# Kernel optimization log

Measured on AMD Instinct MI355X. Metric: run time of the kernel, lower is better.

Reference implementation:

```python
import jax, jax.numpy as jnp
import numpy as np

B, T, IN, OUT, R = 8, 2048, 4096, 4096, 64


def setup_inputs() -> dict:
    key = jax.random.key(0)
    ks = jax.random.split(key, 6)
    x = jax.random.normal(ks[0], (B, T, IN), dtype=jnp.float32)
    weight_main = jax.random.normal(ks[1], (OUT, IN), dtype=jnp.float32) * (1.0 / np.sqrt(IN))
    U = jax.random.normal(ks[2], (OUT, R), dtype=jnp.float32) * 0.02
    S = jax.random.uniform(ks[3], (R,), dtype=jnp.float32)
    V = jax.random.normal(ks[4], (R, IN), dtype=jnp.float32) * 0.02
    bias = jax.random.normal(ks[5], (OUT,), dtype=jnp.float32) * 0.01
    return {"x": x, "weight_main": weight_main, "U": U, "S": S, "V": V, "bias": bias}


def reference(x, weight_main, U, S, V, bias):
    # residual_weight = einsum('ij,j,jk->ik', U, S, V): full [out, in] materialization
    residual_weight = jnp.einsum('ij,j,jk->ik', U, S, V)
    weight = weight_main + residual_weight
    # F.linear: x @ weight.T + bias
    return jnp.einsum('bti,oi->bto', x, weight) + bias
```

## Files before the change

### kernel.cpp

```cpp
#include <hip/hip_runtime.h>
#include <hip/hip_bf16.h>
#include <stdint.h>

#define DI __device__ __forceinline__

typedef __attribute__((ext_vector_type(4))) float f32x4;
typedef __attribute__((ext_vector_type(8))) short bf16x8;
typedef __attribute__((ext_vector_type(4))) short s16x4;

typedef unsigned short ushort_t;

constexpr int M_ = 16384;
constexpr int N_ = 4096;
constexpr int K_ = 4096;
constexpr int R_ = 64;

constexpr int BM = 256, BN = 256, BK = 64;
constexpr int NSEG = 3;
constexpr int NT_SEG = K_ / BK;
constexpr int TOT_T = NSEG * NT_SEG;

DI ushort_t f32_to_bf16_rne(float f) {
    unsigned u = __builtin_bit_cast(unsigned, f);
    u += 0x7FFFu + ((u >> 16) & 1u);
    return (ushort_t)(u >> 16);
}
DI float bf16_to_f32(ushort_t h) {
    return __builtin_bit_cast(float, (unsigned)h << 16);
}

DI void async_cp16(const void* g, void* l) {
    __builtin_amdgcn_global_load_lds(
        (const __attribute__((address_space(1))) unsigned*)g,
        (__attribute__((address_space(3))) unsigned*)l, 16, 0, 0);
}

__global__ __launch_bounds__(256) void k_fold_us(const float* __restrict__ U,
                                                 const float* __restrict__ S,
                                                 float* __restrict__ US) {
    int i = blockIdx.x * 256 + threadIdx.x;
    if (i < N_ * R_) US[i] = U[i] * S[i & (R_ - 1)];
}

__global__ __launch_bounds__(256) void k_fuse_w(const float* __restrict__ WM,
                                                const float* __restrict__ US,
                                                const float* __restrict__ V,
                                                ushort_t* __restrict__ hiW,
                                                ushort_t* __restrict__ loW) {
    __shared__ __align__(16) float sUS[64][68];
    __shared__ __align__(16) float sV[64][128];
    int t = threadIdx.x;
    int n0 = (blockIdx.x >> 5) * 64;
    int k0 = (blockIdx.x & 31) * 128;
#pragma unroll
    for (int j = 0; j < 4; ++j) {
        int f = j * 1024 + t * 4;
        int r = f >> 6, c = f & 63;
        *(f32x4*)&sUS[r][c] = *(const f32x4*)&US[(size_t)(n0 + r) * R_ + c];
    }
#pragma unroll
    for (int j = 0; j < 8; ++j) {
        int f = j * 1024 + t * 4;
        int r = f >> 7, c = f & 127;
        *(f32x4*)&sV[r][c] = *(const f32x4*)&V[(size_t)r * K_ + k0 + c];
    }
    __syncthreads();
    int tn = t >> 5;
    int tk = t & 31;
    float acc[8][4] = {};
    for (int r = 0; r < R_; ++r) {
        f32x4 vv = *(const f32x4*)&sV[r][tk * 4];
#pragma unroll
        for (int a = 0; a < 8; ++a) {
            float u = sUS[tn * 8 + a][r];
#pragma unroll
            for (int c = 0; c < 4; ++c) acc[a][c] += u * vv[c];
        }
    }
#pragma unroll
    for (int a = 0; a < 8; ++a) {
        int n = n0 + tn * 8 + a;
        int k = k0 + tk * 4;
        f32x4 wmv = *(const f32x4*)&WM[(size_t)n * K_ + k];
        s16x4 h4, l4;
#pragma unroll
        for (int c = 0; c < 4; ++c) {
            float w = wmv[c] + acc[a][c];
            ushort_t h = f32_to_bf16_rne(w);
            h4[c] = (short)h;
            l4[c] = (short)f32_to_bf16_rne(w - bf16_to_f32(h));
        }
        *(s16x4*)&hiW[(size_t)n * K_ + k] = h4;
        *(s16x4*)&loW[(size_t)n * K_ + k] = l4;
    }
}

__global__ __launch_bounds__(256) void k_split_x(const float* __restrict__ X,
                                                 ushort_t* __restrict__ hiA,
                                                 ushort_t* __restrict__ loA) {
    size_t i = ((size_t)blockIdx.x * 256 + threadIdx.x) * 8;
    f32x4 a = *(const f32x4*)&X[i];
    f32x4 b = *(const f32x4*)&X[i + 4];
    bf16x8 h, l;
#pragma unroll
    for (int j = 0; j < 4; ++j) {
        ushort_t ha = f32_to_bf16_rne(a[j]);
        ushort_t hb = f32_to_bf16_rne(b[j]);
        h[j]     = (short)ha;
        h[4 + j] = (short)hb;
        l[j]     = (short)f32_to_bf16_rne(a[j] - bf16_to_f32(ha));
        l[4 + j] = (short)f32_to_bf16_rne(b[j] - bf16_to_f32(hb));
    }
    *(bf16x8*)&hiA[i] = h;
    *(bf16x8*)&loA[i] = l;
}

__global__ __launch_bounds__(512, 2) void k_gemm_big(const ushort_t* __restrict__ hiA,
                                                     const ushort_t* __restrict__ loA,
                                                     const ushort_t* __restrict__ hiW,
                                                     const ushort_t* __restrict__ loW,
                                                     const float* __restrict__ bias,
                                                     float* __restrict__ out) {
    __shared__ __align__(16) ushort_t lA[2][BM * BK];
    __shared__ __align__(16) ushort_t lB[2][BN * BK];

    int bid = blockIdx.x;
    int wg  = (bid & 7) * (gridDim.x >> 3) + (bid >> 3);
    int m0  = (wg >> 4) * BM;
    int n0  = (wg & 15) * BN;

    int tid  = threadIdx.x;
    int lane = tid & 63;
    int w    = tid >> 6;
    int wr   = w >> 2;
    int wc   = w & 3;
    int fr   = lane & 15;
    int fq   = lane >> 4;

    f32x4 acc[8][4] = {};

    auto stage = [&](int tau, int bsel) {
        int seg = tau >> 6;
        const ushort_t* As = (seg == 1) ? loA : hiA;
        const ushort_t* Bs = (seg == 2) ? loW : hiW;
        int k0 = (tau & (NT_SEG - 1)) * BK;
        ushort_t* la = lA[bsel];
        ushort_t* lb = lB[bsel];
#pragma unroll
        for (int j = 0; j < 4; ++j) {
            int ci = j * 512 + tid;
            int row = ci >> 3, pc = ci & 7;
            int lc  = pc ^ (row & 7);
            async_cp16(&As[(size_t)(m0 + row) * K_ + k0 + lc * 8], &la[ci * 8]);
        }
#pragma unroll
        for (int j = 0; j < 4; ++j) {
            int ci = j * 512 + tid;
            int row = ci >> 3, pc = ci & 7;
            int lc  = pc ^ (row & 7);
            async_cp16(&Bs[(size_t)(n0 + row) * K_ + k0 + lc * 8], &lb[ci * 8]);
        }
    };

    auto compute = [&](int bsel) {
        const ushort_t* la = lA[bsel];
        const ushort_t* lb = lB[bsel];
#pragma unroll
        for (int ks = 0; ks < 2; ++ks) {
            bf16x8 af[8], bf[4];
#pragma unroll
            for (int i = 0; i < 8; ++i) {
                int row = wr * 128 + i * 16 + fr;
                af[i] = *(const bf16x8*)&la[row * 64 + (((ks * 4 + fq) ^ (row & 7)) << 3)];
            }
#pragma unroll
            for (int j = 0; j < 4; ++j) {
                int row = wc * 64 + j * 16 + fr;
                bf[j] = *(const bf16x8*)&lb[row * 64 + (((ks * 4 + fq) ^ (row & 7)) << 3)];
            }
            __builtin_amdgcn_s_setprio(1);
#pragma unroll
            for (int i = 0; i < 8; ++i)
#pragma unroll
                for (int j = 0; j < 4; ++j)
                    acc[i][j] = __builtin_amdgcn_mfma_f32_16x16x32_bf16(af[i], bf[j], acc[i][j], 0, 0, 0);
            __builtin_amdgcn_s_setprio(0);
        }
    };

    stage(0, 0);
    for (int tau = 0; tau < TOT_T - 1; ++tau) {
        stage(tau + 1, (tau + 1) & 1);
        asm volatile("s_waitcnt vmcnt(8)" ::: "memory");
        __builtin_amdgcn_s_barrier();
        compute(tau & 1);
        asm volatile("" ::: "memory");
        __builtin_amdgcn_s_barrier();
        asm volatile("" ::: "memory");
    }
    asm volatile("s_waitcnt vmcnt(0)" ::: "memory");
    __builtin_amdgcn_s_barrier();
    compute((TOT_T - 1) & 1);

    float bcol[4];
#pragma unroll
    for (int j = 0; j < 4; ++j) bcol[j] = bias[n0 + wc * 64 + j * 16 + fr];
#pragma unroll
    for (int i = 0; i < 8; ++i) {
        int gm = m0 + wr * 128 + i * 16 + fq * 4;
#pragma unroll
        for (int j = 0; j < 4; ++j) {
            int gn = n0 + wc * 64 + j * 16 + fr;
#pragma unroll
            for (int r2 = 0; r2 < 4; ++r2)
                out[(size_t)(gm + r2) * N_ + gn] = acc[i][j][r2] + bcol[j];
        }
    }
}

__global__ __launch_bounds__(256, 2) void k_gemm_small(const float* __restrict__ X,
                                                       const ushort_t* __restrict__ hiW,
                                                       const ushort_t* __restrict__ loW,
                                                       const float* __restrict__ bias,
                                                       float* __restrict__ out) {
    __shared__ __align__(16) ushort_t lA[128 * 64];
    __shared__ __align__(16) ushort_t lB[128 * 64];
    int bid = blockIdx.x;
    int cpx = gridDim.x >> 3;
    int wg  = (bid & 7) * cpx + (bid >> 3);
    constexpr int NBN = N_ / 128;
    int m0 = (wg / NBN) * 128;
    int n0 = (wg % NBN) * 128;
    int tid  = threadIdx.x;
    int lane = tid & 63;
    int w    = tid >> 6;
    int wr   = w >> 1, wc = w & 1;
    int fr   = lane & 15;
    int fq   = lane >> 4;
    f32x4 acc[4][4] = {};
    for (int seg = 0; seg < 3; ++seg) {
        const ushort_t* Bs = (seg == 2) ? loW : hiW;
        bool wantLo = (seg == 1);
        for (int kt = 0; kt < K_ / 64; ++kt) {
            int k0 = kt * 64;
#pragma unroll
            for (int j = 0; j < 4; ++j) {
                int f = j * 2048 + tid * 8;
                int row = f >> 6, col = f & 63;
                async_cp16(&Bs[(size_t)(n0 + row) * K_ + k0 + col], &lB[f]);
            }
#pragma unroll
            for (int j = 0; j < 4; ++j) {
                int f = j * 2048 + tid * 8;
                int row = f >> 6, c = f & 63;
                const float* xp = &X[(size_t)(m0 + row) * K_ + k0 + c];
                f32x4 x0 = *(const f32x4*)xp;
                f32x4 x1 = *(const f32x4*)(xp + 4);
                bf16x8 o;
#pragma unroll
                for (int e = 0; e < 4; ++e) {
                    ushort_t h0 = f32_to_bf16_rne(x0[e]);
                    ushort_t h1 = f32_to_bf16_rne(x1[e]);
                    o[e]     = (short)(wantLo ? f32_to_bf16_rne(x0[e] - bf16_to_f32(h0)) : h0);
                    o[4 + e] = (short)(wantLo ? f32_to_bf16_rne(x1[e] - bf16_to_f32(h1)) : h1);
                }
                *(bf16x8*)&lA[f] = o;
            }
            __syncthreads();
#pragma unroll
            for (int ks = 0; ks < 2; ++ks) {
                bf16x8 af[4], bfv[4];
#pragma unroll
                for (int i = 0; i < 4; ++i) {
                    af[i]  = *(const bf16x8*)&lA[(wr * 64 + i * 16 + fr) * 64 + ks * 32 + fq * 8];
                    bfv[i] = *(const bf16x8*)&lB[(wc * 64 + i * 16 + fr) * 64 + ks * 32 + fq * 8];
                }
#pragma unroll
                for (int i = 0; i < 4; ++i)
#pragma unroll
                    for (int j = 0; j < 4; ++j)
                        acc[i][j] = __builtin_amdgcn_mfma_f32_16x16x32_bf16(af[i], bfv[j], acc[i][j], 0, 0, 0);
            }
            __syncthreads();
        }
    }
    float bcol[4];
#pragma unroll
    for (int j = 0; j < 4; ++j) bcol[j] = bias[n0 + wc * 64 + j * 16 + fr];
#pragma unroll
    for (int i = 0; i < 4; ++i) {
        int gm = m0 + wr * 64 + i * 16 + fq * 4;
#pragma unroll
        for (int j = 0; j < 4; ++j) {
            int gn = n0 + wc * 64 + j * 16 + fr;
#pragma unroll
            for (int r2 = 0; r2 < 4; ++r2)
                out[(size_t)(gm + r2) * N_ + gn] = acc[i][j][r2] + bcol[j];
        }
    }
}

__global__ __launch_bounds__(256) void k_naive(const float* __restrict__ X,
                                               const float* __restrict__ WM,
                                               const float* __restrict__ U,
                                               const float* __restrict__ S,
                                               const float* __restrict__ V,
                                               const float* __restrict__ bias,
                                               float* __restrict__ out) {
    __shared__ __align__(16) float sX[64][68];
    __shared__ __align__(16) float sW[64][68];
    __shared__ __align__(16) float sV[64][68];
    int t = threadIdx.x;
    int m0 = (blockIdx.x >> 6) * 64;
    int n0 = (blockIdx.x & 63) * 64;
    int tm = t >> 4, tn = t & 15;
    float acc[4][4] = {}, pacc[4][4] = {};
    for (int kc = 0; kc < K_ / 64; ++kc) {
        __syncthreads();
#pragma unroll
        for (int j = 0; j < 4; ++j) {
            int f = j * 1024 + t * 4;
            int r = f >> 6, c = f & 63;
            *(f32x4*)&sX[r][c] = *(const f32x4*)&X[(size_t)(m0 + r) * K_ + kc * 64 + c];
            *(f32x4*)&sW[r][c] = *(const f32x4*)&WM[(size_t)(n0 + r) * K_ + kc * 64 + c];
            *(f32x4*)&sV[r][c] = *(const f32x4*)&V[(size_t)r * K_ + kc * 64 + c];
        }
        __syncthreads();
        for (int k4 = 0; k4 < 16; ++k4) {
            f32x4 xa[4], wb[4], vb[4];
#pragma unroll
            for (int a = 0; a < 4; ++a) xa[a] = *(const f32x4*)&sX[tm * 4 + a][k4 * 4];
#pragma unroll
            for (int b = 0; b < 4; ++b) {
                wb[b] = *(const f32x4*)&sW[tn * 4 + b][k4 * 4];
                vb[b] = *(const f32x4*)&sV[tn * 4 + b][k4 * 4];
            }
#pragma unroll
            for (int a = 0; a < 4; ++a)
#pragma unroll
                for (int b = 0; b < 4; ++b)
#pragma unroll
                    for (int e = 0; e < 4; ++e) {
                        acc[a][b]  += xa[a][e] * wb[b][e];
                        pacc[a][b] += xa[a][e] * vb[b][e];
                    }
        }
    }
    __syncthreads();
#pragma unroll
    for (int j = 0; j < 4; ++j) {
        int f = j * 1024 + t * 4;
        int nl = f >> 6, r = f & 63;
        f32x4 uu = *(const f32x4*)&U[(size_t)(n0 + nl) * R_ + r];
        f32x4 ss = *(const f32x4*)&S[r];
        f32x4 us = uu * ss;
        *(f32x4*)&sV[nl][r] = us;
    }
#pragma unroll
    for (int a = 0; a < 4; ++a)
#pragma unroll
        for (int b = 0; b < 4; ++b) sW[tm * 4 + a][tn * 4 + b] = pacc[a][b];
    __syncthreads();
#pragma unroll
    for (int a = 0; a < 4; ++a)
#pragma unroll
        for (int b = 0; b < 4; ++b) {
            float s2 = acc[a][b];
            for (int r = 0; r < R_; ++r) s2 += sW[tm * 4 + a][r] * sV[tn * 4 + b][r];
            out[(size_t)(m0 + tm * 4 + a) * N_ + n0 + tn * 4 + b] = s2 + bias[n0 + tn * 4 + b];
        }
}

extern "C" void kernel_launch(void* const* d_in, const int* in_sizes, int n_in,
                              void* d_out, int out_size, void* d_ws, size_t ws_size,
                              hipStream_t stream) {
    const float* x    = (const float*)d_in[0];
    const float* wm   = (const float*)d_in[1];
    const float* U    = (const float*)d_in[2];
    const float* S    = (const float*)d_in[3];
    const float* V    = (const float*)d_in[4];
    const float* bias = (const float*)d_in[5];
    float* out = (float*)d_out;

    const size_t szA  = (size_t)M_ * K_ * 2;
    const size_t szW  = (size_t)N_ * K_ * 2;
    const size_t szUS = (size_t)N_ * R_ * 4;

    if (ws_size >= 2 * szA + 2 * szW + szUS) {
        ushort_t* hiA = (ushort_t*)d_ws;
        ushort_t* loA = (ushort_t*)((char*)d_ws + szA);
        ushort_t* hiW = (ushort_t*)((char*)d_ws + 2 * szA);
        ushort_t* loW = (ushort_t*)((char*)d_ws + 2 * szA + szW);
        float*    US  = (float*)((char*)d_ws + 2 * szA + 2 * szW);
        k_fold_us<<<dim3((N_ * R_ + 255) / 256), dim3(256), 0, stream>>>(U, S, US);
        k_fuse_w<<<dim3((N_ / 64) * (K_ / 128)), dim3(256), 0, stream>>>(wm, US, V, hiW, loW);
        k_split_x<<<dim3(M_ * K_ / 2048), dim3(256), 0, stream>>>(x, hiA, loA);
        k_gemm_big<<<dim3((M_ / BM) * (N_ / BN)), dim3(512), 0, stream>>>(
            hiA, loA, hiW, loW, bias, out);
    } else if (ws_size >= 2 * szW + szUS) {
        ushort_t* hiW = (ushort_t*)d_ws;
        ushort_t* loW = (ushort_t*)((char*)d_ws + szW);
        float*    US  = (float*)((char*)d_ws + 2 * szW);
        k_fold_us<<<dim3((N_ * R_ + 255) / 256), dim3(256), 0, stream>>>(U, S, US);
        k_fuse_w<<<dim3((N_ / 64) * (K_ / 128)), dim3(256), 0, stream>>>(wm, US, V, hiW, loW);
        k_gemm_small<<<dim3((M_ / 128) * (N_ / 128)), dim3(256), 0, stream>>>(
            x, hiW, loW, bias, out);
    } else {
        k_naive<<<dim3((M_ / 64) * (N_ / 64)), dim3(256), 0, stream>>>(x, wm, U, S, V, bias, out);
    }
}
```

Measured before the change: 2.142 ms.

## Restructure big GEMM main loop into 8-phase interleaved load/MFMA schedule

Replaces the simple double-buffered stage/compute loop with an eight-phase schedule. Each phase loads half a tile's worth of A or B for the next K-step, reads a quarter of the LDS fragments, and runs a 4x2 MFMA sub-block at raised priority between barriers. The goal is to spread global-to-LDS copies and LDS reads across the MFMA work so memory latency hides behind matrix math, in the style of ping-pong GEMM schedules. The cost is many more barriers per tile and fragile manual waitcnt accounting. The wraparound prefetch at the end also issues redundant loads for the first tile.

```diff
diff --git a/kernel.cpp b/kernel.cpp
--- a/kernel.cpp
+++ b/kernel.cpp
@@ -34,6 +34,15 @@
         (const __attribute__((address_space(1))) unsigned*)g,
         (__attribute__((address_space(3))) unsigned*)l, 16, 0, 0);
 }
+
+#define BAR() do { asm volatile("" ::: "memory"); \
+                   __builtin_amdgcn_s_barrier(); \
+                   asm volatile("" ::: "memory"); } while (0)
+#define MID() do { BAR(); \
+                   asm volatile("s_waitcnt lgkmcnt(0)" ::: "memory"); \
+                   __builtin_amdgcn_sched_barrier(0); \
+                   __builtin_amdgcn_s_setprio(1); } while (0)
+#define ENDP() do { __builtin_amdgcn_s_setprio(0); BAR(); } while (0)
 
 __global__ __launch_bounds__(256) void k_fold_us(const float* __restrict__ U,
                                                  const float* __restrict__ S,
@@ -115,7 +124,7 @@
     *(bf16x8*)&loA[i] = l;
 }
 
-__global__ __launch_bounds__(512, 2) void k_gemm_big(const ushort_t* __restrict__ hiA,
+__global__ __launch_bounds__(512, 2) void k_gemm_8ph(const ushort_t* __restrict__ hiA,
                                                      const ushort_t* __restrict__ loA,
                                                      const ushort_t* __restrict__ hiW,
                                                      const ushort_t* __restrict__ loW,
@@ -139,68 +148,169 @@
 
     f32x4 acc[8][4] = {};
 
-    auto stage = [&](int tau, int bsel) {
+    auto stageA = [&](int tau, int h) {
         int seg = tau >> 6;
         const ushort_t* As = (seg == 1) ? loA : hiA;
+        int k0 = (tau & (NT_SEG - 1)) * BK;
+        ushort_t* dst = &lA[tau & 1][h * (128 * 64)];
+#pragma unroll
+        for (int j = 0; j < 2; ++j) {
+            int ci  = j * 512 + tid;
+            int row = ci >> 3, pc = ci & 7;
+            int lc  = pc ^ (row & 7);
+            async_cp16(&As[(size_t)(m0 + h * 128 + row) * K_ + k0 + lc * 8], &dst[ci * 8]);
+        }
+    };
+    auto stageB = [&](int tau, int h) {
+        int seg = tau >> 6;
         const ushort_t* Bs = (seg == 2) ? loW : hiW;
         int k0 = (tau & (NT_SEG - 1)) * BK;
-        ushort_t* la = lA[bsel];
-        ushort_t* lb = lB[bsel];
-#pragma unroll
-        for (int j = 0; j < 4; ++j) {
-            int ci = j * 512 + tid;
+        ushort_t* dst = &lB[tau & 1][h * (128 * 64)];
+#pragma unroll
+        for (int j = 0; j < 2; ++j) {
+            int ci  = j * 512 + tid;
             int row = ci >> 3, pc = ci & 7;
             int lc  = pc ^ (row & 7);
-            async_cp16(&As[(size_t)(m0 + row) * K_ + k0 + lc * 8], &la[ci * 8]);
-        }
-#pragma unroll
-        for (int j = 0; j < 4; ++j) {
-            int ci = j * 512 + tid;
-            int row = ci >> 3, pc = ci & 7;
-            int lc  = pc ^ (row & 7);
-            async_cp16(&Bs[(size_t)(n0 + row) * K_ + k0 + lc * 8], &lb[ci * 8]);
+            async_cp16(&Bs[(size_t)(n0 + h * 128 + row) * K_ + k0 + lc * 8], &dst[ci * 8]);
         }
     };
-
-    auto compute = [&](int bsel) {
-        const ushort_t* la = lA[bsel];
-        const ushort_t* lb = lB[bsel];
-#pragma unroll
-        for (int ks = 0; ks < 2; ++ks) {
-            bf16x8 af[8], bf[4];
-#pragma unroll
-            for (int i = 0; i < 8; ++i) {
-                int row = wr * 128 + i * 16 + fr;
-                af[i] = *(const bf16x8*)&la[row * 64 + (((ks * 4 + fq) ^ (row & 7)) << 3)];
-            }
-#pragma unroll
-            for (int j = 0; j < 4; ++j) {
-                int row = wc * 64 + j * 16 + fr;
-                bf[j] = *(const bf16x8*)&lb[row * 64 + (((ks * 4 + fq) ^ (row & 7)) << 3)];
-            }
-            __builtin_amdgcn_s_setprio(1);
-#pragma unroll
-            for (int i = 0; i < 8; ++i)
-#pragma unroll
-                for (int j = 0; j < 4; ++j)
-                    acc[i][j] = __builtin_amdgcn_mfma_f32_16x16x32_bf16(af[i], bf[j], acc[i][j], 0, 0, 0);
-            __builtin_amdgcn_s_setprio(0);
-        }
+    auto rdA = [&](const ushort_t* la, int i, int ks) -> bf16x8 {
+        int row = wr * 128 + i * 16 + fr;
+        return *(const bf16x8*)&la[row * 64 + (((ks * 4 + fq) ^ (row & 7)) << 3)];
     };
-
-    stage(0, 0);
-    for (int tau = 0; tau < TOT_T - 1; ++tau) {
-        stage(tau + 1, (tau + 1) & 1);
-        asm volatile("s_waitcnt vmcnt(8)" ::: "memory");
-        __builtin_amdgcn_s_barrier();
-        compute(tau & 1);
-        asm volatile("" ::: "memory");
-        __builtin_amdgcn_s_barrier();
-        asm volatile("" ::: "memory");
-    }
+    auto rdB = [&](const ushort_t* lb, int j, int ks) -> bf16x8 {
+        int row = wc * 64 + j * 16 + fr;
+        return *(const bf16x8*)&lb[row * 64 + (((ks * 4 + fq) ^ (row & 7)) << 3)];
+    };
+
+    bf16x8 aF[4][2];
+    bf16x8 bE[2][2];
+    bf16x8 bO[2][2];
+
+    stageB(0, 0); stageB(0, 1); stageA(0, 0); stageA(0, 1);
+    stageB(1, 0); stageB(1, 1);
+    asm volatile("s_waitcnt vmcnt(4)" ::: "memory");
+    BAR();
+
+    const ushort_t* la0 = lA[0]; const ushort_t* lb0 = lB[0];
+    const ushort_t* la1 = lA[1]; const ushort_t* lb1 = lB[1];
+
+    constexpr int NIT = TOT_T / 2;
+    for (int it = 0; it < NIT; ++it) {
+        int to = 2 * it + 1;
+        int ne = (2 * it + 2) % TOT_T;
+        int no = (2 * it + 3) % TOT_T;
+
+#pragma unroll
+        for (int i = 0; i < 4; ++i) { aF[i][0] = rdA(la0, i, 0); aF[i][1] = rdA(la0, i, 1); }
+#pragma unroll
+        for (int j = 0; j < 2; ++j) { bE[j][0] = rdB(lb0, j, 0); bE[j][1] = rdB(lb0, j, 1); }
+        stageA(to, 0);
+        asm volatile("s_waitcnt lgkmcnt(8)" ::: "memory");
+        MID();
+#pragma unroll
+        for (int i = 0; i < 4; ++i)
+#pragma unroll
+            for (int j = 0; j < 2; ++j)
+#pragma unroll
+                for (int ks = 0; ks < 2; ++ks)
+                    acc[i][j] = __builtin_amdgcn_mfma_f32_16x16x32_bf16(aF[i][ks], bE[j][ks], acc[i][j], 0, 0, 0);
+        ENDP();
+
+#pragma unroll
+        for (int j = 0; j < 2; ++j) { bO[j][0] = rdB(lb0, 2 + j, 0); bO[j][1] = rdB(lb0, 2 + j, 1); }
+        stageA(to, 1);
+        MID();
+#pragma unroll
+        for (int i = 0; i < 4; ++i)
+#pragma unroll
+            for (int j = 0; j < 2; ++j)
+#pragma unroll
+                for (int ks = 0; ks < 2; ++ks)
+                    acc[i][2 + j] = __builtin_amdgcn_mfma_f32_16x16x32_bf16(aF[i][ks], bO[j][ks], acc[i][2 + j], 0, 0, 0);
+        ENDP();
+
+#pragma unroll
+        for (int i = 0; i < 4; ++i) { aF[i][0] = rdA(la0, 4 + i, 0); aF[i][1] = rdA(la0, 4 + i, 1); }
+        stageB(ne, 0);
+        MID();
+#pragma unroll
+        for (int i = 0; i < 4; ++i)
+#pragma unroll
+            for (int j = 0; j < 2; ++j)
+#pragma unroll
+                for (int ks = 0; ks < 2; ++ks)
+                    acc[4 + i][2 + j] = __builtin_amdgcn_mfma_f32_16x16x32_bf16(aF[i][ks], bO[j][ks], acc[4 + i][2 + j], 0, 0, 0);
+        ENDP();
+
+        stageB(ne, 1);
+        asm volatile("s_waitcnt vmcnt(4)" ::: "memory");
+        MID();
+#pragma unroll
+        for (int i = 0; i < 4; ++i)
+#pragma unroll
+            for (int j = 0; j < 2; ++j)
+#pragma unroll
+                for (int ks = 0; ks < 2; ++ks)
+                    acc[4 + i][j] = __builtin_amdgcn_mfma_f32_16x16x32_bf16(aF[i][ks], bE[j][ks], acc[4 + i][j], 0, 0, 0);
+        ENDP();
+
+#pragma unroll
+        for (int i = 0; i < 4; ++i) { aF[i][0] = rdA(la1, i, 0); aF[i][1] = rdA(la1, i, 1); }
+#pragma unroll
+        for (int j = 0; j < 2; ++j) { bE[j][0] = rdB(lb1, j, 0); bE[j][1] = rdB(lb1, j, 1); }
+        stageA(ne, 0);
+        asm volatile("s_waitcnt lgkmcnt(8)" ::: "memory");
+        MID();
+#pragma unroll
+        for (int i = 0; i < 4; ++i)
+#pragma unroll
+            for (int j = 0; j < 2; ++j)
+#pragma unroll
+                for (int ks = 0; ks < 2; ++ks)
+                    acc[i][j] = __builtin_amdgcn_mfma_f32_16x16x32_bf16(aF[i][ks], bE[j][ks], acc[i][j], 0, 0, 0);
+        ENDP();
+
+#pragma unroll
+        for (int j = 0; j < 2; ++j) { bO[j][0] = rdB(lb1, 2 + j, 0); bO[j][1] = rdB(lb1, 2 + j, 1); }
+        stageA(ne, 1);
+        MID();
+#pragma unroll
+        for (int i = 0; i < 4; ++i)
+#pragma unroll
+            for (int j = 0; j < 2; ++j)
+#pragma unroll
+                for (int ks = 0; ks < 2; ++ks)
+                    acc[i][2 + j] = __builtin_amdgcn_mfma_f32_16x16x32_bf16(aF[i][ks], bO[j][ks], acc[i][2 + j], 0, 0, 0);
+        ENDP();
+
+#pragma unroll
+        for (int i = 0; i < 4; ++i) { aF[i][0] = rdA(la1, 4 + i, 0); aF[i][1] = rdA(la1, 4 + i, 1); }
+        stageB(no, 0);
+        MID();
+#pragma unroll
+        for (int i = 0; i < 4; ++i)
+#pragma unroll
+            for (int j = 0; j < 2; ++j)
+#pragma unroll
+                for (int ks = 0; ks < 2; ++ks)
+                    acc[4 + i][2 + j] = __builtin_amdgcn_mfma_f32_16x16x32_bf16(aF[i][ks], bO[j][ks], acc[4 + i][2 + j], 0, 0, 0);
+        ENDP();
+
+        stageB(no, 1);
+        asm volatile("s_waitcnt vmcnt(4)" ::: "memory");
+        MID();
+#pragma unroll
+        for (int i = 0; i < 4; ++i)
+#pragma unroll
+            for (int j = 0; j < 2; ++j)
+#pragma unroll
+                for (int ks = 0; ks < 2; ++ks)
+                    acc[4 + i][j] = __builtin_amdgcn_mfma_f32_16x16x32_bf16(aF[i][ks], bE[j][ks], acc[4 + i][j], 0, 0, 0);
+        ENDP();
+    }
+
     asm volatile("s_waitcnt vmcnt(0)" ::: "memory");
-    __builtin_amdgcn_s_barrier();
-    compute((TOT_T - 1) & 1);
 
     float bcol[4];
 #pragma unroll
@@ -395,7 +505,7 @@
         k_fold_us<<<dim3((N_ * R_ + 255) / 256), dim3(256), 0, stream>>>(U, S, US);
         k_fuse_w<<<dim3((N_ / 64) * (K_ / 128)), dim3(256), 0, stream>>>(wm, US, V, hiW, loW);
         k_split_x<<<dim3(M_ * K_ / 2048), dim3(256), 0, stream>>>(x, hiA, loA);
-        k_gemm_big<<<dim3((M_ / BM) * (N_ / BN)), dim3(512), 0, stream>>>(
+        k_gemm_8ph<<<dim3((M_ / BM) * (N_ / BN)), dim3(512), 0, stream>>>(
             hiA, loA, hiW, loW, bias, out);
     } else if (ws_size >= 2 * szW + szUS) {
         ushort_t* hiW = (ushort_t*)d_ws;
```

Result: faster. 1.873 ms (-12.6%).
